# Performance work log

Hardware: AMD Instinct MI355X
Metric: run time of the kernel (lower is better)

## Reference

```python
import jax, jax.numpy as jnp
import numpy as np

B, S, D, DFF, E, TOPK = 4, 2048, 1024, 4096, 8, 2


def setup_inputs() -> dict:
    key = jax.random.key(0)
    ks = jax.random.split(key, 7)
    scale_r = 1.0 / np.sqrt(D)
    scale_1 = 1.0 / np.sqrt(D)
    scale_2 = 1.0 / np.sqrt(DFF)
    return {
        "x": jax.random.normal(ks[0], (B, S, D), dtype=jnp.float32),
        "Wr": jax.random.normal(ks[1], (D, E), dtype=jnp.float32) * scale_r,
        "br": jnp.zeros((E,), dtype=jnp.float32),
        "W1": jax.random.normal(ks[2], (E, D, DFF), dtype=jnp.float32) * scale_1,
        "b1": jnp.zeros((E, DFF), dtype=jnp.float32),
        "W2": jax.random.normal(ks[3], (E, DFF, D), dtype=jnp.float32) * scale_2,
        "b2": jnp.zeros((E, D), dtype=jnp.float32),
    }


def reference(x, Wr, br, W1, b1, W2, b2):
    # Router: per-token logits over experts. [B,S,E]
    router_logits = jnp.einsum("bsd,de->bse", x, Wr) + br
    # top-k expert selection, softmax over the k selected logits (matches
    # torch.topk + F.softmax(dim=-1) on the topk values).
    topk_w, topk_idx = jax.lax.top_k(router_logits, TOPK)  # [B,S,K]
    topk_w = jax.nn.softmax(topk_w, axis=-1)
    # Dense per-expert gates: gates[b,s,e] = sum_k topk_w[b,s,k] * [idx==e]
    one_hot = jax.nn.one_hot(topk_idx, E, dtype=x.dtype)  # [B,S,K,E]
    gates = jnp.einsum("bsk,bske->bse", topk_w, one_hot)  # [B,S,E]
    # Per-expert FFN compute + weighted scatter-add combine.
    out = jnp.zeros_like(x)
    for e in range(E):  # small fixed loop over experts
        h = jax.nn.gelu(jnp.einsum("bsd,df->bsf", x, W1[e]) + b1[e])
        y = jnp.einsum("bsf,fd->bsd", h, W2[e]) + b2[e]
        out = out + gates[:, :, e, None] * y
    return out
```

## Files before the change

kernel.cpp:

```cpp
#include <hip/hip_runtime.h>
#include <cstdio>
#include <cstdint>

#define TOKENS 8192
#define DMODEL 1024
#define DFF    4096
#define NEXP   8
#define TCAP   8192
#define ROWS   16384

typedef __attribute__((ext_vector_type(8))) short short8;
typedef __attribute__((ext_vector_type(4))) float f32x4;

__device__ __forceinline__ unsigned short f2bf(float f){
  unsigned u = __builtin_bit_cast(unsigned, f);
  u += 0x7FFFu + ((u >> 16) & 1u);
  return (unsigned short)(u >> 16);
}

__device__ __forceinline__ void async16(void* lds, const void* g){
  __builtin_amdgcn_global_load_lds((const __attribute__((address_space(1))) void*)g,
                                   (__attribute__((address_space(3))) void*)lds,
                                   16, 0, 0);
}

__device__ __forceinline__ float gelu_tanh(float x){
  float t = 0.7978845608028654f * (x + 0.044715f * x * x * x);
  float e = __expf(2.0f * t);
  float th = 1.0f - 2.0f / (e + 1.0f);
  return 0.5f * x * (1.0f + th);
}

__global__ __launch_bounds__(256) void router_kernel(
    const float* __restrict__ x, const float* __restrict__ Wr, const float* __restrict__ br,
    int* __restrict__ cnt, int* __restrict__ list,
    int* __restrict__ tk_e, int* __restrict__ tk_s, float* __restrict__ tk_g)
{
  int t = blockIdx.x * 4 + (threadIdx.x >> 6);
  int lane = threadIdx.x & 63;
  const float* xr = x + (size_t)t * DMODEL;
  float acc[8];
#pragma unroll
  for (int e = 0; e < 8; e++) acc[e] = 0.f;
#pragma unroll
  for (int j = 0; j < 16; j++){
    int d = lane + 64 * j;
    float xv = xr[d];
    const f32x4* w = (const f32x4*)(Wr + (size_t)d * 8);
    f32x4 w0 = w[0], w1 = w[1];
    acc[0] += xv * w0.x; acc[1] += xv * w0.y; acc[2] += xv * w0.z; acc[3] += xv * w0.w;
    acc[4] += xv * w1.x; acc[5] += xv * w1.y; acc[6] += xv * w1.z; acc[7] += xv * w1.w;
  }
#pragma unroll
  for (int e = 0; e < 8; e++){
    float v = acc[e];
#pragma unroll
    for (int o = 32; o > 0; o >>= 1) v += __shfl_xor(v, o, 64);
    acc[e] = v;
  }
  if (lane == 0){
    float lg[8];
#pragma unroll
    for (int e = 0; e < 8; e++) lg[e] = acc[e] + br[e];
    int i0 = 0; float v0 = lg[0];
#pragma unroll
    for (int e = 1; e < 8; e++) if (lg[e] > v0){ v0 = lg[e]; i0 = e; }
    int i1 = -1; float v1 = -3.4e38f;
#pragma unroll
    for (int e = 0; e < 8; e++) if (e != i0 && lg[e] > v1){ v1 = lg[e]; i1 = e; }
    float ew = __expf(v1 - v0);
    float w1 = ew / (1.f + ew);
    float w0 = 1.f - w1;
    int s0 = atomicAdd(&cnt[i0], 1);
    int s1 = atomicAdd(&cnt[i1], 1);
    list[i0 * TCAP + s0] = t;
    list[i1 * TCAP + s1] = t;
    tk_e[2*t]   = i0; tk_s[2*t]   = s0; tk_g[2*t]   = w0;
    tk_e[2*t+1] = i1; tk_s[2*t+1] = s1; tk_g[2*t+1] = w1;
  }
}

__global__ void scan_kernel(const int* __restrict__ cnt, int* __restrict__ off){
  if (threadIdx.x == 0 && blockIdx.x == 0){
    int o = 0;
    for (int e = 0; e < NEXP; e++){ off[e] = o; o += cnt[e]; }
    off[NEXP] = o;
  }
}

__global__ __launch_bounds__(256) void xconv_kernel(const float* __restrict__ x,
                                                    unsigned short* __restrict__ xb)
{
  size_t i = (size_t)(blockIdx.x * 256 + threadIdx.x) * 8;
  f32x4 a = *(const f32x4*)(x + i);
  f32x4 b = *(const f32x4*)(x + i + 4);
  short8 o;
  o[0]=(short)f2bf(a.x); o[1]=(short)f2bf(a.y); o[2]=(short)f2bf(a.z); o[3]=(short)f2bf(a.w);
  o[4]=(short)f2bf(b.x); o[5]=(short)f2bf(b.y); o[6]=(short)f2bf(b.z); o[7]=(short)f2bf(b.w);
  *(short8*)(xb + i) = o;
}

__global__ __launch_bounds__(256) void transpose_kernel(const float* __restrict__ src,
                                                        unsigned short* __restrict__ dst,
                                                        int R, int C)
{
  __shared__ float tile[32][33];
  int e = blockIdx.z;
  size_t ebase = (size_t)e * R * C;
  int c0 = blockIdx.x * 32;
  int r0 = blockIdx.y * 32;
  int tx = threadIdx.x & 31;
  int ty = threadIdx.x >> 5;
  const float* s = src + ebase;
  unsigned short* d = dst + ebase;
#pragma unroll
  for (int i = 0; i < 4; i++)
    tile[ty + 8*i][tx] = s[(size_t)(r0 + ty + 8*i) * C + c0 + tx];
  __syncthreads();
#pragma unroll
  for (int i = 0; i < 4; i++)
    d[(size_t)(c0 + ty + 8*i) * R + r0 + tx] = f2bf(tile[tx][ty + 8*i]);
}

template<int MODE>
__global__ __launch_bounds__(256, 2) void gemm_kernel(
    const unsigned short* __restrict__ A0, int lda,
    const int* __restrict__ list,
    const unsigned short* __restrict__ B0, int ldb, long strideBe,
    const int* __restrict__ cnt, const int* __restrict__ off,
    int K,
    unsigned short* __restrict__ hout, float* __restrict__ yout, int ldout,
    const float* __restrict__ bias, int nbase, int accum)
{
  int e = blockIdx.z;
  int cnte = cnt[e];
  int bm = blockIdx.y;
  if (bm * 128 >= cnte) return;
  int bn = blockIdx.x;
  int offe = off[e];

  __shared__ unsigned short smem[2][128 * 64 * 2];

  int tid  = threadIdx.x;
  int lane = tid & 63;
  int wav  = tid >> 6;
  int slot = tid & 7;

  const unsigned short* aptr[4];
  const unsigned short* bptr[4];
  const unsigned short* Be = B0 + (size_t)e * strideBe;
#pragma unroll
  for (int c = 0; c < 4; c++){
    int r  = bm * 128 + c * 32 + (tid >> 3);
    int rr = min(r, cnte - 1);
    long arow = list ? (long)list[(size_t)e * TCAP + rr] : (long)(offe + rr);
    aptr[c] = A0 + (size_t)arow * lda + slot * 8;
    int n = bn * 128 + c * 32 + (tid >> 3);
    bptr[c] = Be + (size_t)n * ldb + slot * 8;
  }

  auto stage = [&](int buf, int k0){
    char* Ad = (char*)smem + buf * 32768;
    char* Bd = Ad + 16384;
#pragma unroll
    for (int c = 0; c < 4; c++){
      async16(Ad + c * 4096 + wav * 1024, aptr[c] + k0);
      async16(Bd + c * 4096 + wav * 1024, bptr[c] + k0);
    }
  };

  f32x4 acc[4][4] = {};

  int wm = wav >> 1, wn = wav & 1;
  int l15 = lane & 15, l4 = lane >> 4;

  stage(0, 0);
  __syncthreads();
  int cur = 0;
  for (int k0 = 0; k0 < K; k0 += 64){
    if (k0 + 64 < K) stage(cur ^ 1, k0 + 64);
    char* Ab = (char*)smem + cur * 32768;
    char* Bb = Ab + 16384;
#pragma unroll
    for (int kk = 0; kk < 2; kk++){
      short8 a[4], b[4];
      int k8 = kk * 4 + l4;
#pragma unroll
      for (int m = 0; m < 4; m++){
        int row = wm * 64 + m * 16 + l15;
        a[m] = *(const short8*)(Ab + row * 128 + (k8 << 4));
      }
#pragma unroll
      for (int n = 0; n < 4; n++){
        int col = wn * 64 + n * 16 + l15;
        b[n] = *(const short8*)(Bb + col * 128 + (k8 << 4));
      }
#pragma unroll
      for (int m = 0; m < 4; m++)
#pragma unroll
        for (int n = 0; n < 4; n++)
          acc[m][n] = __builtin_amdgcn_mfma_f32_16x16x32_bf16(a[m], b[n], acc[m][n], 0, 0, 0);
    }
    __syncthreads();
    cur ^= 1;
  }

#pragma unroll
  for (int m = 0; m < 4; m++){
#pragma unroll
    for (int n = 0; n < 4; n++){
      int coll = wn * 64 + n * 16 + l15;
#pragma unroll
      for (int q = 0; q < 4; q++){
        int rowl = wm * 64 + m * 16 + l4 * 4 + q;
        int r = bm * 128 + rowl;
        if (r < cnte){
          float v = acc[m][n][q];
          size_t orow = (size_t)(offe + r);
          int col = bn * 128 + coll;
          if (MODE == 0){
            v += bias[(size_t)e * DFF + nbase + col];
            v = gelu_tanh(v);
            hout[orow * (size_t)ldout + col] = f2bf(v);
          } else {
            size_t oi = orow * (size_t)ldout + col;
            if (accum) v += yout[oi];
            yout[oi] = v;
          }
        }
      }
    }
  }
}

__global__ __launch_bounds__(256) void combine_kernel(
    const float* __restrict__ y, const float* __restrict__ b2,
    const int* __restrict__ off, const int* __restrict__ tk_e,
    const int* __restrict__ tk_s, const float* __restrict__ tk_g,
    float* __restrict__ out)
{
  int t = blockIdx.x;
  int d = threadIdx.x * 4;
  int e0 = tk_e[2*t],  e1 = tk_e[2*t+1];
  int s0 = tk_s[2*t],  s1 = tk_s[2*t+1];
  float g0 = tk_g[2*t], g1 = tk_g[2*t+1];
  size_t r0 = (size_t)(off[e0] + s0) * DMODEL + d;
  size_t r1 = (size_t)(off[e1] + s1) * DMODEL + d;
  f32x4 v0 = *(const f32x4*)(y + r0);
  f32x4 v1 = *(const f32x4*)(y + r1);
  f32x4 c0 = *(const f32x4*)(b2 + (size_t)e0 * DMODEL + d);
  f32x4 c1 = *(const f32x4*)(b2 + (size_t)e1 * DMODEL + d);
  f32x4 o  = g0 * (v0 + c0) + g1 * (v1 + c1);
  *(f32x4*)(out + (size_t)t * DMODEL + d) = o;
}

extern "C" void kernel_launch(void* const* d_in, const int* in_sizes, int n_in,
                              void* d_out, int out_size, void* d_ws, size_t ws_size,
                              hipStream_t stream)
{
  const float* x  = (const float*)d_in[0];
  const float* Wr = (const float*)d_in[1];
  const float* br = (const float*)d_in[2];
  const float* W1 = (const float*)d_in[3];
  const float* b1 = (const float*)d_in[4];
  const float* W2 = (const float*)d_in[5];
  const float* b2 = (const float*)d_in[6];
  float* out = (float*)d_out;

  char* ws = (char*)d_ws;
  size_t o = 0;
  auto carve = [&](size_t bytes) -> char* {
    char* p = ws + o;
    o += (bytes + 255) & ~(size_t)255;
    return p;
  };
  int* cnt   = (int*)carve(NEXP * 4);
  int* off   = (int*)carve((NEXP + 1) * 4);
  int* list  = (int*)carve((size_t)NEXP * TCAP * 4);
  int* tk_e  = (int*)carve(TOKENS * 2 * 4);
  int* tk_s  = (int*)carve(TOKENS * 2 * 4);
  float* tk_g = (float*)carve(TOKENS * 2 * 4);
  unsigned short* xb  = (unsigned short*)carve((size_t)TOKENS * DMODEL * 2);
  unsigned short* W1t = (unsigned short*)carve((size_t)NEXP * DFF * DMODEL * 2);
  unsigned short* W2t = (unsigned short*)carve((size_t)NEXP * DFF * DMODEL * 2);
  float* y = (float*)carve((size_t)ROWS * DMODEL * 4);
  size_t used_base = o;

  int nchunk = 0;
  for (int nc = 1; nc <= 8; nc <<= 1){
    size_t need = used_base + (size_t)ROWS * (DFF / nc) * 2 + 256;
    if (need <= ws_size){ nchunk = nc; break; }
  }
  if (!nchunk){
    fprintf(stderr, "kernel_launch: ws too small (%zu bytes, need >= %zu)\n",
            ws_size, used_base + (size_t)ROWS * (DFF / 8) * 2 + 256);
    return;
  }
  int dffc = DFF / nchunk;
  unsigned short* h = (unsigned short*)carve((size_t)ROWS * dffc * 2);

  hipMemsetAsync(cnt, 0, NEXP * 4, stream);
  router_kernel<<<TOKENS / 4, 256, 0, stream>>>(x, Wr, br, cnt, list, tk_e, tk_s, tk_g);
  scan_kernel<<<1, 64, 0, stream>>>(cnt, off);
  xconv_kernel<<<(TOKENS * DMODEL / 8) / 256, 256, 0, stream>>>(x, xb);
  transpose_kernel<<<dim3(DFF / 32, DMODEL / 32, NEXP), 256, 0, stream>>>(W1, W1t, DMODEL, DFF);
  transpose_kernel<<<dim3(DMODEL / 32, DFF / 32, NEXP), 256, 0, stream>>>(W2, W2t, DFF, DMODEL);

  for (int c = 0; c < nchunk; c++){
    gemm_kernel<0><<<dim3(dffc / 128, 64, NEXP), 256, 0, stream>>>(
        xb, DMODEL, list,
        W1t + (size_t)c * dffc * DMODEL, DMODEL, (long)DFF * DMODEL,
        cnt, off, DMODEL,
        h, nullptr, dffc,
        b1, c * dffc, 0);
    gemm_kernel<1><<<dim3(DMODEL / 128, 64, NEXP), 256, 0, stream>>>(
        h, dffc, nullptr,
        W2t + (size_t)c * dffc, DFF, (long)DFF * DMODEL,
        cnt, off, dffc,
        nullptr, y, DMODEL,
        nullptr, 0, c > 0);
  }
  combine_kernel<<<TOKENS, 256, 0, stream>>>(y, b2, off, tk_e, tk_s, tk_g, out);
}
```

Before: 845.4 us.

## Enlarge expert GEMM tile to 256x128 with 512 threads and triple-buffered async loads

The grouped expert GEMM now uses 8 waves per block and a 256-row M tile, so each B tile is reused across twice as many token rows. The two-stage double buffer with full __syncthreads becomes a three-stage LDS ring. Explicit s_waitcnt vmcnt counts keep two global-to-LDS stages in flight behind a single barrier per K step. The costs are a single block per CU, about 144 KB of LDS, and a grid that only covers 4096 rows per expert, which assumes no expert receives more tokens than that.

```diff
diff --git a/kernel.cpp b/kernel.cpp
--- a/kernel.cpp
+++ b/kernel.cpp
@@ -123,7 +123,7 @@
 }
 
 template<int MODE>
-__global__ __launch_bounds__(256, 2) void gemm_kernel(
+__global__ __launch_bounds__(512, 1) void gemm_kernel(
     const unsigned short* __restrict__ A0, int lda,
     const int* __restrict__ list,
     const unsigned short* __restrict__ B0, int ldb, long strideBe,
@@ -135,11 +135,11 @@
   int e = blockIdx.z;
   int cnte = cnt[e];
   int bm = blockIdx.y;
-  if (bm * 128 >= cnte) return;
+  if (bm * 256 >= cnte) return;
   int bn = blockIdx.x;
   int offe = off[e];
 
-  __shared__ unsigned short smem[2][128 * 64 * 2];
+  __shared__ unsigned short smem[3][(256 + 128) * 64];
 
   int tid  = threadIdx.x;
   int lane = tid & 63;
@@ -147,26 +147,30 @@
   int slot = tid & 7;
 
   const unsigned short* aptr[4];
-  const unsigned short* bptr[4];
+  const unsigned short* bptr[2];
   const unsigned short* Be = B0 + (size_t)e * strideBe;
 #pragma unroll
   for (int c = 0; c < 4; c++){
-    int r  = bm * 128 + c * 32 + (tid >> 3);
+    int r  = bm * 256 + c * 64 + (tid >> 3);
     int rr = min(r, cnte - 1);
     long arow = list ? (long)list[(size_t)e * TCAP + rr] : (long)(offe + rr);
     aptr[c] = A0 + (size_t)arow * lda + slot * 8;
-    int n = bn * 128 + c * 32 + (tid >> 3);
+  }
+#pragma unroll
+  for (int c = 0; c < 2; c++){
+    int n = bn * 128 + c * 64 + (tid >> 3);
     bptr[c] = Be + (size_t)n * ldb + slot * 8;
   }
 
   auto stage = [&](int buf, int k0){
-    char* Ad = (char*)smem + buf * 32768;
-    char* Bd = Ad + 16384;
-#pragma unroll
-    for (int c = 0; c < 4; c++){
-      async16(Ad + c * 4096 + wav * 1024, aptr[c] + k0);
-      async16(Bd + c * 4096 + wav * 1024, bptr[c] + k0);
-    }
+    char* Ad = (char*)smem + (size_t)buf * 49152;
+    char* Bd = Ad + 32768;
+#pragma unroll
+    for (int c = 0; c < 4; c++)
+      async16(Ad + c * 8192 + wav * 1024, aptr[c] + k0);
+#pragma unroll
+    for (int c = 0; c < 2; c++)
+      async16(Bd + c * 8192 + wav * 1024, bptr[c] + k0);
   };
 
   f32x4 acc[4][4] = {};
@@ -174,13 +178,17 @@
   int wm = wav >> 1, wn = wav & 1;
   int l15 = lane & 15, l4 = lane >> 4;
 
+  int NT = K >> 6;
   stage(0, 0);
-  __syncthreads();
+  stage(1, 64);
   int cur = 0;
-  for (int k0 = 0; k0 < K; k0 += 64){
-    if (k0 + 64 < K) stage(cur ^ 1, k0 + 64);
-    char* Ab = (char*)smem + cur * 32768;
-    char* Bb = Ab + 16384;
+  for (int t = 0; t < NT; t++){
+    if (t < NT - 1) asm volatile("s_waitcnt vmcnt(6)" ::: "memory");
+    else            asm volatile("s_waitcnt vmcnt(0)" ::: "memory");
+    __builtin_amdgcn_s_barrier();
+    if (t + 2 < NT) stage((cur + 2) % 3, (t + 2) << 6);
+    char* Ab = (char*)smem + (size_t)cur * 49152;
+    char* Bb = Ab + 32768;
 #pragma unroll
     for (int kk = 0; kk < 2; kk++){
       short8 a[4], b[4];
@@ -201,29 +209,26 @@
         for (int n = 0; n < 4; n++)
           acc[m][n] = __builtin_amdgcn_mfma_f32_16x16x32_bf16(a[m], b[n], acc[m][n], 0, 0, 0);
     }
-    __syncthreads();
-    cur ^= 1;
+    cur = (cur + 1) % 3;
   }
 
 #pragma unroll
   for (int m = 0; m < 4; m++){
 #pragma unroll
     for (int n = 0; n < 4; n++){
-      int coll = wn * 64 + n * 16 + l15;
+      int coll = bn * 128 + wn * 64 + n * 16 + l15;
 #pragma unroll
       for (int q = 0; q < 4; q++){
-        int rowl = wm * 64 + m * 16 + l4 * 4 + q;
-        int r = bm * 128 + rowl;
+        int r = bm * 256 + wm * 64 + m * 16 + l4 * 4 + q;
         if (r < cnte){
           float v = acc[m][n][q];
           size_t orow = (size_t)(offe + r);
-          int col = bn * 128 + coll;
           if (MODE == 0){
-            v += bias[(size_t)e * DFF + nbase + col];
+            v += bias[(size_t)e * DFF + nbase + coll];
             v = gelu_tanh(v);
-            hout[orow * (size_t)ldout + col] = f2bf(v);
+            hout[orow * (size_t)ldout + coll] = f2bf(v);
           } else {
-            size_t oi = orow * (size_t)ldout + col;
+            size_t oi = orow * (size_t)ldout + coll;
             if (accum) v += yout[oi];
             yout[oi] = v;
           }
@@ -307,13 +312,13 @@
   transpose_kernel<<<dim3(DMODEL / 32, DFF / 32, NEXP), 256, 0, stream>>>(W2, W2t, DFF, DMODEL);
 
   for (int c = 0; c < nchunk; c++){
-    gemm_kernel<0><<<dim3(dffc / 128, 64, NEXP), 256, 0, stream>>>(
+    gemm_kernel<0><<<dim3(dffc / 128, 16, NEXP), 512, 0, stream>>>(
         xb, DMODEL, list,
         W1t + (size_t)c * dffc * DMODEL, DMODEL, (long)DFF * DMODEL,
         cnt, off, DMODEL,
         h, nullptr, dffc,
         b1, c * dffc, 0);
-    gemm_kernel<1><<<dim3(DMODEL / 128, 64, NEXP), 256, 0, stream>>>(
+    gemm_kernel<1><<<dim3(DMODEL / 128, 16, NEXP), 512, 0, stream>>>(
         h, dffc, nullptr,
         W2t + (size_t)c * dffc, DFF, (long)DFF * DMODEL,
         cnt, off, dffc,
```

Measured after the change: 929.5 us. 10.0% more time.

## Swizzle LDS tiles in GEMM and issue all fragment reads before MFMAs

Applied to the files above, without the earlier changes.

The source column of each 16-byte global-to-LDS load is XOR-swizzled by row, and the fragment reads apply the same swizzle, to remove LDS bank conflicts on the 128-byte-stride row layout. The inner loop is reorganised to issue all eight ds_read_b128 loads up front using inline asm, wait partially with lgkmcnt(8), run the first 16 MFMAs, then wait for the rest. This is meant to overlap LDS latency with matrix math. Explicit waitcnt and sched_barrier constrain compiler scheduling, and the inline-asm reads bypass compiler dependency tracking.

```diff
diff --git a/kernel.cpp b/kernel.cpp
--- a/kernel.cpp
+++ b/kernel.cpp
@@ -22,6 +22,14 @@
   __builtin_amdgcn_global_load_lds((const __attribute__((address_space(1))) void*)g,
                                    (__attribute__((address_space(3))) void*)lds,
                                    16, 0, 0);
+}
+
+__device__ __forceinline__ short8 lds_read_b128(const char* p){
+  short8 r;
+  asm volatile("ds_read_b128 %0, %1"
+               : "=v"(r)
+               : "v"((const __attribute__((address_space(3))) char*)p));
+  return r;
 }
 
 __device__ __forceinline__ float gelu_tanh(float x){
@@ -144,7 +152,7 @@
   int tid  = threadIdx.x;
   int lane = tid & 63;
   int wav  = tid >> 6;
-  int slot = tid & 7;
+  int sslot = (tid & 7) ^ ((tid >> 3) & 7);
 
   const unsigned short* aptr[4];
   const unsigned short* bptr[4];
@@ -154,13 +162,13 @@
     int r  = bm * 128 + c * 32 + (tid >> 3);
     int rr = min(r, cnte - 1);
     long arow = list ? (long)list[(size_t)e * TCAP + rr] : (long)(offe + rr);
-    aptr[c] = A0 + (size_t)arow * lda + slot * 8;
+    aptr[c] = A0 + (size_t)arow * lda + sslot * 8;
     int n = bn * 128 + c * 32 + (tid >> 3);
-    bptr[c] = Be + (size_t)n * ldb + slot * 8;
+    bptr[c] = Be + (size_t)n * ldb + sslot * 8;
   }
 
   auto stage = [&](int buf, int k0){
-    char* Ad = (char*)smem + buf * 32768;
+    char* Ad = (char*)smem + (size_t)buf * 32768;
     char* Bd = Ad + 16384;
 #pragma unroll
     for (int c = 0; c < 4; c++){
@@ -173,34 +181,47 @@
 
   int wm = wav >> 1, wn = wav & 1;
   int l15 = lane & 15, l4 = lane >> 4;
-
+  int swz = l15 & 7;
+
+  int NT = K >> 6;
   stage(0, 0);
   __syncthreads();
   int cur = 0;
-  for (int k0 = 0; k0 < K; k0 += 64){
-    if (k0 + 64 < K) stage(cur ^ 1, k0 + 64);
-    char* Ab = (char*)smem + cur * 32768;
+  for (int t = 0; t < NT; t++){
+    if (t + 1 < NT) stage(cur ^ 1, (t + 1) << 6);
+    char* Ab = (char*)smem + (size_t)cur * 32768;
     char* Bb = Ab + 16384;
-#pragma unroll
-    for (int kk = 0; kk < 2; kk++){
-      short8 a[4], b[4];
-      int k8 = kk * 4 + l4;
-#pragma unroll
-      for (int m = 0; m < 4; m++){
-        int row = wm * 64 + m * 16 + l15;
-        a[m] = *(const short8*)(Ab + row * 128 + (k8 << 4));
-      }
-#pragma unroll
-      for (int n = 0; n < 4; n++){
-        int col = wn * 64 + n * 16 + l15;
-        b[n] = *(const short8*)(Bb + col * 128 + (k8 << 4));
-      }
-#pragma unroll
-      for (int m = 0; m < 4; m++)
-#pragma unroll
-        for (int n = 0; n < 4; n++)
-          acc[m][n] = __builtin_amdgcn_mfma_f32_16x16x32_bf16(a[m], b[n], acc[m][n], 0, 0, 0);
-    }
+    const char* Arow = Ab + (wm * 64 + l15) * 128;
+    const char* Brow = Bb + (wn * 64 + l15) * 128;
+    int ks0 = (l4 ^ swz) << 4;
+    int ks1 = ((4 + l4) ^ swz) << 4;
+
+    short8 a0[4], b0[4], a1[4], b1[4];
+#pragma unroll
+    for (int m = 0; m < 4; m++) a0[m] = lds_read_b128(Arow + m * 2048 + ks0);
+#pragma unroll
+    for (int n = 0; n < 4; n++) b0[n] = lds_read_b128(Brow + n * 2048 + ks0);
+#pragma unroll
+    for (int m = 0; m < 4; m++) a1[m] = lds_read_b128(Arow + m * 2048 + ks1);
+#pragma unroll
+    for (int n = 0; n < 4; n++) b1[n] = lds_read_b128(Brow + n * 2048 + ks1);
+
+    asm volatile("s_waitcnt lgkmcnt(8)" ::: "memory");
+    __builtin_amdgcn_sched_barrier(0);
+#pragma unroll
+    for (int m = 0; m < 4; m++)
+#pragma unroll
+      for (int n = 0; n < 4; n++)
+        acc[m][n] = __builtin_amdgcn_mfma_f32_16x16x32_bf16(a0[m], b0[n], acc[m][n], 0, 0, 0);
+
+    asm volatile("s_waitcnt lgkmcnt(0)" ::: "memory");
+    __builtin_amdgcn_sched_barrier(0);
+#pragma unroll
+    for (int m = 0; m < 4; m++)
+#pragma unroll
+      for (int n = 0; n < 4; n++)
+        acc[m][n] = __builtin_amdgcn_mfma_f32_16x16x32_bf16(a1[m], b1[n], acc[m][n], 0, 0, 0);
+
     __syncthreads();
     cur ^= 1;
   }
@@ -209,21 +230,19 @@
   for (int m = 0; m < 4; m++){
 #pragma unroll
     for (int n = 0; n < 4; n++){
-      int coll = wn * 64 + n * 16 + l15;
+      int coll = bn * 128 + wn * 64 + n * 16 + l15;
 #pragma unroll
       for (int q = 0; q < 4; q++){
-        int rowl = wm * 64 + m * 16 + l4 * 4 + q;
-        int r = bm * 128 + rowl;
+        int r = bm * 128 + wm * 64 + m * 16 + l4 * 4 + q;
         if (r < cnte){
           float v = acc[m][n][q];
           size_t orow = (size_t)(offe + r);
-          int col = bn * 128 + coll;
           if (MODE == 0){
-            v += bias[(size_t)e * DFF + nbase + col];
+            v += bias[(size_t)e * DFF + nbase + coll];
             v = gelu_tanh(v);
-            hout[orow * (size_t)ldout + col] = f2bf(v);
+            hout[orow * (size_t)ldout + coll] = f2bf(v);
           } else {
-            size_t oi = orow * (size_t)ldout + col;
+            size_t oi = orow * (size_t)ldout + coll;
             if (accum) v += yout[oi];
             yout[oi] = v;
           }
@@ -307,13 +326,13 @@
   transpose_kernel<<<dim3(DMODEL / 32, DFF / 32, NEXP), 256, 0, stream>>>(W2, W2t, DFF, DMODEL);
 
   for (int c = 0; c < nchunk; c++){
-    gemm_kernel<0><<<dim3(dffc / 128, 64, NEXP), 256, 0, stream>>>(
+    gemm_kernel<0><<<dim3(dffc / 128, TCAP / 128, NEXP), 256, 0, stream>>>(
         xb, DMODEL, list,
         W1t + (size_t)c * dffc * DMODEL, DMODEL, (long)DFF * DMODEL,
         cnt, off, DMODEL,
         h, nullptr, dffc,
         b1, c * dffc, 0);
-    gemm_kernel<1><<<dim3(DMODEL / 128, 64, NEXP), 256, 0, stream>>>(
+    gemm_kernel<1><<<dim3(DMODEL / 128, TCAP / 128, NEXP), 256, 0, stream>>>(
         h, dffc, nullptr,
         W2t + (size_t)c * dffc, DFF, (long)DFF * DMODEL,
         cnt, off, dffc,
```

Result: faster. 826.7 us (-2.2%).
